# Kernel tuning notes

Measured on AMD Instinct MI355X. Metric: run time of the kernel, lower is better.

Reference implementation:

```python
import jax, jax.numpy as jnp
import numpy as np

HEADS, OUT = 3, 12          # num_heads=3, out_size = output_size*his_num = 12
NEG_SLOPE = 0.2             # PyG GATConv default leaky_relu slope


def gat_layer(y, src, dst, W, a_src, a_dst, bias, concat):
    """One PyG-style GATConv (self-loops already appended to src/dst)."""
    N = y.shape[0]
    h = (y @ W.T).reshape(N, HEADS, OUT)              # [N,H,O]
    al_s = jnp.sum(h * a_src, axis=-1)                # [N,H]
    al_d = jnp.sum(h * a_dst, axis=-1)                # [N,H]
    e = jax.nn.leaky_relu(al_s[src] + al_d[dst], NEG_SLOPE)   # [E,H]
    m = jax.ops.segment_max(e, dst, num_segments=N)
    m = jnp.where(jnp.isfinite(m), m, 0.0)            # guard empty segments
    p = jnp.exp(e - m[dst])
    s = jax.ops.segment_sum(p, dst, num_segments=N)
    alpha = p / (s[dst] + 1e-16)                      # segment softmax
    out = jax.ops.segment_sum(h[src] * alpha[:, :, None], dst, num_segments=N)
    out = out.reshape(N, HEADS * OUT) if concat else out.mean(axis=1)
    return out + bias


def setup_inputs() -> dict:
    key = jax.random.key(0)
    ks = jax.random.split(key, 24)
    B, N, T, C = 1, 50000, 12, 2
    E = 800000
    x = jax.random.normal(ks[0], (B, N, T, C), dtype=jnp.float32)
    edge_index = jax.random.randint(ks[1], (2, E), 0, N, dtype=jnp.int32)
    sc = 0.1
    d = {"x": x, "edge_index": edge_index}
    # layer 0: in=24, layers 1,2: in=36 (concat), layer 3: in=36, concat=False
    ins = [24, 36, 36, 36]
    for l in range(4):
        d[f"W{l}"] = jax.random.normal(ks[2 + 5 * l], (HEADS * OUT, ins[l]), jnp.float32) * sc
        d[f"a_src{l}"] = jax.random.normal(ks[3 + 5 * l], (HEADS, OUT), jnp.float32) * sc
        d[f"a_dst{l}"] = jax.random.normal(ks[4 + 5 * l], (HEADS, OUT), jnp.float32) * sc
        d[f"b{l}"] = jnp.zeros((HEADS * OUT,) if l < 3 else (OUT,), jnp.float32)
    d["lin1_w"] = jax.random.normal(ks[22], (12, 12), jnp.float32) * sc
    d["lin1_b"] = jnp.zeros((12,), jnp.float32)
    d["lin2_w"] = jax.random.normal(ks[23], (6, 12), jnp.float32) * sc
    d["lin2_b"] = jnp.zeros((6,), jnp.float32)
    return d


def reference(x, edge_index, W0, a_src0, a_dst0, b0, W1, a_src1, a_dst1, b1,
              W2, a_src2, a_dst2, b2, W3, a_src3, a_dst3, b3,
              lin1_w, lin1_b, lin2_w, lin2_b):
    b, n, t, c = x.shape
    N = b * n
    y = x.reshape(N, t * c)
    loop = jnp.arange(N, dtype=edge_index.dtype)      # PyG add_self_loops=True
    src = jnp.concatenate([edge_index[0], loop])
    dst = jnp.concatenate([edge_index[1], loop])
    y = jax.nn.relu(gat_layer(y, src, dst, W0, a_src0, a_dst0, b0, True))
    y = jax.nn.relu(gat_layer(y, src, dst, W1, a_src1, a_dst1, b1, True))
    y = jax.nn.relu(gat_layer(y, src, dst, W2, a_src2, a_dst2, b2, True))
    y = gat_layer(y, src, dst, W3, a_src3, a_dst3, b3, False)
    y = y @ lin1_w.T + lin1_b
    y = y @ lin2_w.T + lin2_b
    return y.reshape(b, n, -1)
```

## Files before the change

kernel.cpp:

```cpp
#include <hip/hip_runtime.h>
#include <hip/hip_fp16.h>

#define HEADS 3
#define OUT   12
#define HO    36
#define ROWH  40
#define NMAX  50000
#define CAP   64
#define NPB   28

__device__ __align__(16) unsigned short g_h16A[NMAX * ROWH];
__device__ __align__(16) unsigned short g_h16B[NMAX * ROWH];
__device__ float g_aldA[NMAX * HEADS], g_aldB[NMAX * HEADS];
__device__ int g_pos  [NMAX];
__device__ unsigned short g_elist[NMAX * CAP];

__global__ void scatter_transform24_kernel(const int* __restrict__ ei,
                                           const float* __restrict__ x,
                                           const float* __restrict__ W,
                                           const float* __restrict__ As,
                                           const float* __restrict__ Ad,
                                           int E, int N,
                                           int scatterStart, int scatterBlocks) {
    __shared__ float sW[HO * 24];
    __shared__ float sAs[HO], sAd[HO];
    if (blockIdx.x >= scatterStart) {
        int group = blockIdx.x & 7;
        int bi    = (blockIdx.x - scatterStart) >> 3;
        int range = (N + 7) >> 3;
        int lo = group * range;
        int hi = lo + range; if (hi > N) hi = N;
        int stride = (scatterBlocks >> 3) * 256;
        for (int t = bi * 256 + threadIdx.x; t < E + N; t += stride) {
            int dst = (t < E) ? ei[E + t] : (t - E);
            if (dst < lo || dst >= hi) continue;
            int src = (t < E) ? ei[t] : dst;
            int k = atomicAdd(&g_pos[dst], 1);
            if (k < CAP) g_elist[dst * CAP + k] = (unsigned short)src;
        }
        return;
    }
    for (int i = threadIdx.x; i < HO * 24; i += blockDim.x) sW[i] = W[i];
    if (threadIdx.x < HO) { sAs[threadIdx.x] = As[threadIdx.x]; sAd[threadIdx.x] = Ad[threadIdx.x]; }
    __syncthreads();
    int n = blockIdx.x * blockDim.x + threadIdx.x;
    if (n >= N) return;

    float yv[24];
    const float4* xp = (const float4*)(x + n * 24);
    for (int i = 0; i < 6; ++i) *(float4*)(yv + 4 * i) = xp[i];

    float hr[HO];
    float als[HEADS] = {0.f, 0.f, 0.f};
    float ald[HEADS] = {0.f, 0.f, 0.f};
    for (int ho = 0; ho < HO; ++ho) {
        float acc = 0.f;
#pragma unroll
        for (int k = 0; k < 24; ++k) acc += yv[k] * sW[ho * 24 + k];
        hr[ho] = acc;
        int hd = ho / OUT;
        als[hd] += acc * sAs[ho];
        ald[hd] += acc * sAd[ho];
    }
    unsigned short hp[ROWH];
#pragma unroll
    for (int i = 0; i < HO; ++i) hp[i] = __half_as_ushort(__float2half_rn(hr[i]));
#pragma unroll
    for (int hd = 0; hd < HEADS; ++hd)
        hp[HO + hd] = __half_as_ushort(__float2half_rn(als[hd]));
    hp[ROWH - 1] = 0;
    uint4* dp = (uint4*)(g_h16A + (size_t)n * ROWH);
    const uint4* sp = (const uint4*)hp;
#pragma unroll
    for (int i = 0; i < 5; ++i) dp[i] = sp[i];
    for (int hd = 0; hd < HEADS; ++hd)
        g_aldA[n * HEADS + hd] = ald[hd];
}

__device__ __forceinline__ void gather_row16(int n, int q, int hd,
                                             const unsigned short* __restrict__ hin,
                                             float ald, float4& acc, float& wsum) {
    const unsigned short* row = g_elist + n * CAP;
    int deg = g_pos[n]; if (deg > CAP) deg = CAP;
    const int4* rp = (const int4*)row;
#pragma unroll
    for (int c = 0; c < 4; ++c) {
        if (c * 8 >= deg) break;
        int4 r = rp[c];
#pragma unroll
        for (int j = 0; j < 8; ++j) {
            int s = c * 8 + j;
            if (s < deg) {
                int w2 = (&r.x)[j >> 1];
                int src = (j & 1) ? ((w2 >> 16) & 0xFFFF) : (w2 & 0xFFFF);
                const unsigned short* hrow = hin + (size_t)src * ROWH;
                float als = __half2float(*(const __half*)(hrow + HO + hd));
                float e = als + ald;
                e = (e > 0.f) ? e : 0.2f * e;
                float w = __expf(e);
                wsum += w;
                uint2 hv = *(const uint2*)(hrow + q * 4);
                float2 f0 = __half22float2(*(__half2*)&hv.x);
                float2 f1 = __half22float2(*(__half2*)&hv.y);
                acc.x += w * f0.x; acc.y += w * f0.y;
                acc.z += w * f1.x; acc.w += w * f1.y;
            }
        }
    }
    for (int s = 32; s < deg; ++s) {
        int src = row[s];
        const unsigned short* hrow = hin + (size_t)src * ROWH;
        float als = __half2float(*(const __half*)(hrow + HO + hd));
        float e = als + ald;
        e = (e > 0.f) ? e : 0.2f * e;
        float w = __expf(e);
        wsum += w;
        uint2 hv = *(const uint2*)(hrow + q * 4);
        float2 f0 = __half22float2(*(__half2*)&hv.x);
        float2 f1 = __half22float2(*(__half2*)&hv.y);
        acc.x += w * f0.x; acc.y += w * f0.y;
        acc.z += w * f1.x; acc.w += w * f1.y;
    }
}

__global__ void gather_transform_kernel(const float* __restrict__ bias,
                                        const float* __restrict__ W,
                                        const float* __restrict__ As,
                                        const float* __restrict__ Ad,
                                        int N, int par) {
    const unsigned short* hin = par ? g_h16B : g_h16A;
    const float* aldi = par ? g_aldB : g_aldA;
    unsigned short* hout = par ? g_h16A : g_h16B;
    float* aldo = par ? g_aldA : g_aldB;

    __shared__ float sW[HO * 37];
    __shared__ float sAs[HO], sAd[HO], sB[HO];
    __shared__ float sy[NPB * HO];
    __shared__ float spals[NPB * 9], spald[NPB * 9];

    for (int i = threadIdx.x; i < HO * 36; i += 256) {
        int r = i / 36, c = i - r * 36;
        sW[r * 37 + c] = W[i];
    }
    if (threadIdx.x < HO) {
        sAs[threadIdx.x] = As[threadIdx.x];
        sAd[threadIdx.x] = Ad[threadIdx.x];
        sB[threadIdx.x]  = bias[threadIdx.x];
    }
    __syncthreads();

    int local = threadIdx.x;
    int nodeL = local / 9;
    int q     = local - nodeL * 9;
    int n     = blockIdx.x * NPB + nodeL;
    bool active = (local < NPB * 9) && (n < N);

    if (active) {
        int hd = q / 3;
        float ald = aldi[n * HEADS + hd];
        float4 acc = {0.f, 0.f, 0.f, 0.f};
        float wsum = 0.f;
        gather_row16(n, q, hd, hin, ald, acc, wsum);
        float inv = 1.f / (wsum + 1e-16f);
        float4 v;
        v.x = acc.x * inv + sB[q * 4 + 0];
        v.y = acc.y * inv + sB[q * 4 + 1];
        v.z = acc.z * inv + sB[q * 4 + 2];
        v.w = acc.w * inv + sB[q * 4 + 3];
        v.x = v.x > 0.f ? v.x : 0.f; v.y = v.y > 0.f ? v.y : 0.f;
        v.z = v.z > 0.f ? v.z : 0.f; v.w = v.w > 0.f ? v.w : 0.f;
        *(float4*)(sy + nodeL * HO + q * 4) = v;
    }
    __syncthreads();

    if (active) {
        const float* yv = sy + nodeL * HO;
        float a0 = 0.f, a1 = 0.f, a2 = 0.f, a3 = 0.f;
        const float* w0 = sW + (q * 4 + 0) * 37;
        const float* w1 = sW + (q * 4 + 1) * 37;
        const float* w2 = sW + (q * 4 + 2) * 37;
        const float* w3 = sW + (q * 4 + 3) * 37;
#pragma unroll
        for (int k = 0; k < 36; ++k) {
            float y = yv[k];
            a0 += y * w0[k]; a1 += y * w1[k];
            a2 += y * w2[k]; a3 += y * w3[k];
        }
        __half2 h01 = __floats2half2_rn(a0, a1);
        __half2 h23 = __floats2half2_rn(a2, a3);
        uint2 st;
        st.x = *(unsigned int*)&h01;
        st.y = *(unsigned int*)&h23;
        *(uint2*)(hout + (size_t)n * ROWH + q * 4) = st;
        int r0 = q * 4;
        spals[nodeL * 9 + q] = a0 * sAs[r0] + a1 * sAs[r0 + 1] + a2 * sAs[r0 + 2] + a3 * sAs[r0 + 3];
        spald[nodeL * 9 + q] = a0 * sAd[r0] + a1 * sAd[r0 + 1] + a2 * sAd[r0 + 2] + a3 * sAd[r0 + 3];
    }
    __syncthreads();

    if (active && q < HEADS) {
        float als = spals[nodeL * 9 + q * 3] + spals[nodeL * 9 + q * 3 + 1] + spals[nodeL * 9 + q * 3 + 2];
        float ald = spald[nodeL * 9 + q * 3] + spald[nodeL * 9 + q * 3 + 1] + spald[nodeL * 9 + q * 3 + 2];
        hout[(size_t)n * ROWH + HO + q] = __half_as_ushort(__float2half_rn(als));
        aldo[n * HEADS + q] = ald;
    }
}

__global__ void gather3_finalize_kernel(const float* __restrict__ b3,
                                        const float* __restrict__ lin1_w,
                                        const float* __restrict__ lin1_b,
                                        const float* __restrict__ lin2_w,
                                        const float* __restrict__ lin2_b,
                                        float* __restrict__ out, int N) {
    __shared__ float sv[NPB * HO];
    __shared__ float sl1[144], sl2[72], sl1b[12], sl2b[6], sb3[12];
    if (threadIdx.x < 144) sl1[threadIdx.x] = lin1_w[threadIdx.x];
    if (threadIdx.x < 72)  sl2[threadIdx.x] = lin2_w[threadIdx.x];
    if (threadIdx.x < 12)  { sl1b[threadIdx.x] = lin1_b[threadIdx.x]; sb3[threadIdx.x] = b3[threadIdx.x]; }
    if (threadIdx.x < 6)   sl2b[threadIdx.x] = lin2_b[threadIdx.x];

    int local = threadIdx.x;
    int nodeL = local / 9;
    int q     = local - nodeL * 9;
    int n     = blockIdx.x * NPB + nodeL;
    if (local < NPB * 9 && n < N) {
        int hd = q / 3;
        float ald = g_aldB[n * HEADS + hd];
        float4 acc = {0.f, 0.f, 0.f, 0.f};
        float wsum = 0.f;
        gather_row16(n, q, hd, g_h16B, ald, acc, wsum);
        float inv = 1.f / (wsum + 1e-16f);
        float* s = sv + nodeL * HO + q * 4;
        s[0] = acc.x * inv; s[1] = acc.y * inv;
        s[2] = acc.z * inv; s[3] = acc.w * inv;
    }
    __syncthreads();
    if (local < NPB) {
        int n2 = blockIdx.x * NPB + local;
        if (n2 < N) {
            g_pos[n2] = 0;
            const float* vv = sv + local * HO;
            float v[12];
            for (int o = 0; o < OUT; ++o)
                v[o] = (vv[o] + vv[12 + o] + vv[24 + o]) * (1.f / 3.f) + sb3[o];
            float t1[12];
            for (int i = 0; i < 12; ++i) {
                float a = sl1b[i];
                for (int o = 0; o < 12; ++o) a += v[o] * sl1[i * 12 + o];
                t1[i] = a;
            }
            for (int j = 0; j < 6; ++j) {
                float a = sl2b[j];
                for (int i = 0; i < 12; ++i) a += t1[i] * sl2[j * 12 + i];
                out[n2 * 6 + j] = a;
            }
        }
    }
}

extern "C" void kernel_launch(void* const* d_in, const int* in_sizes, int n_in,
                              void* d_out, int out_size, void* d_ws, size_t ws_size,
                              hipStream_t stream) {
    if (n_in < 22 || d_out == nullptr) return;

    const float* x  = (const float*)d_in[0];
    const int*   ei = (const int*)d_in[1];
    int N = in_sizes[0] / 24;
    int E = in_sizes[1] / 2;
    if (N > NMAX) N = NMAX;

    const float* W[4], *As[4], *Ad[4], *B[4];
    for (int l = 0; l < 4; ++l) {
        W[l]  = (const float*)d_in[2 + 4 * l];
        As[l] = (const float*)d_in[3 + 4 * l];
        Ad[l] = (const float*)d_in[4 + 4 * l];
        B[l]  = (const float*)d_in[5 + 4 * l];
    }
    const float* lin1_w = (const float*)d_in[18];
    const float* lin1_b = (const float*)d_in[19];
    const float* lin2_w = (const float*)d_in[20];
    const float* lin2_b = (const float*)d_in[21];
    float* out = (float*)d_out;

    const int BLK = 256;
    const int nodeBlocks = (N + BLK - 1) / BLK;
    const int scatterStart = ((nodeBlocks + 7) / 8) * 8;
    const int edgeBlocks = (E + N + BLK - 1) / BLK;
    const int scatterBlocks = ((edgeBlocks + 7) / 8) * 8;
    const int fuseBlocks = (N + NPB - 1) / NPB;

    scatter_transform24_kernel<<<scatterStart + scatterBlocks, BLK, 0, stream>>>(
        ei, x, W[0], As[0], Ad[0], E, N, scatterStart, scatterBlocks);
    gather_transform_kernel<<<fuseBlocks, BLK, 0, stream>>>(B[0], W[1], As[1], Ad[1], N, 0);
    gather_transform_kernel<<<fuseBlocks, BLK, 0, stream>>>(B[1], W[2], As[2], Ad[2], N, 1);
    gather_transform_kernel<<<fuseBlocks, BLK, 0, stream>>>(B[2], W[3], As[3], Ad[3], N, 0);
    gather3_finalize_kernel<<<fuseBlocks, BLK, 0, stream>>>(
        B[3], lin1_w, lin1_b, lin2_w, lin2_b, out, N);
}
```

Measured before the change: 227.1 us.

## Sort nodes by degree into a permutation to balance gather work

```diff
diff --git a/kernel.cpp b/kernel.cpp
--- a/kernel.cpp
+++ b/kernel.cpp
@@ -14,19 +14,21 @@
 __device__ float g_aldA[NMAX * HEADS], g_aldB[NMAX * HEADS];
 __device__ int g_pos  [NMAX];
 __device__ unsigned short g_elist[NMAX * CAP];
+__device__ int g_perm [NMAX];
+__device__ int g_dh   [CAP + 1];
+__device__ int g_dcur [CAP + 1];
 
 __global__ void scatter_transform24_kernel(const int* __restrict__ ei,
                                            const float* __restrict__ x,
                                            const float* __restrict__ W,
                                            const float* __restrict__ As,
                                            const float* __restrict__ Ad,
-                                           int E, int N,
-                                           int scatterStart, int scatterBlocks) {
+                                           int E, int N, int scatterBlocks) {
     __shared__ float sW[HO * 24];
     __shared__ float sAs[HO], sAd[HO];
-    if (blockIdx.x >= scatterStart) {
+    if (blockIdx.x < scatterBlocks) {
         int group = blockIdx.x & 7;
-        int bi    = (blockIdx.x - scatterStart) >> 3;
+        int bi    = blockIdx.x >> 3;
         int range = (N + 7) >> 3;
         int lo = group * range;
         int hi = lo + range; if (hi > N) hi = N;
@@ -43,7 +45,7 @@
     for (int i = threadIdx.x; i < HO * 24; i += blockDim.x) sW[i] = W[i];
     if (threadIdx.x < HO) { sAs[threadIdx.x] = As[threadIdx.x]; sAd[threadIdx.x] = Ad[threadIdx.x]; }
     __syncthreads();
-    int n = blockIdx.x * blockDim.x + threadIdx.x;
+    int n = (blockIdx.x - scatterBlocks) * blockDim.x + threadIdx.x;
     if (n >= N) return;
 
     float yv[24];
@@ -75,6 +77,30 @@
     for (int i = 0; i < 5; ++i) dp[i] = sp[i];
     for (int hd = 0; hd < HEADS; ++hd)
         g_aldA[n * HEADS + hd] = ald[hd];
+}
+
+__global__ void degree_hist_kernel(int N) {
+    if (threadIdx.x <= CAP) g_dcur[threadIdx.x] = 0;
+    for (int n = blockIdx.x * blockDim.x + threadIdx.x; n < N;
+         n += gridDim.x * blockDim.x) {
+        int d = g_pos[n]; if (d > CAP) d = CAP;
+        atomicAdd(&g_dh[d], 1);
+    }
+}
+
+__global__ void perm_place_kernel(int N) {
+    __shared__ int sbase[CAP + 1];
+    if (threadIdx.x == 0) {
+        int acc = 0;
+        for (int b = CAP; b >= 0; --b) { sbase[b] = acc; acc += g_dh[b]; }
+    }
+    __syncthreads();
+    for (int n = blockIdx.x * blockDim.x + threadIdx.x; n < N;
+         n += gridDim.x * blockDim.x) {
+        int d = g_pos[n]; if (d > CAP) d = CAP;
+        int off = atomicAdd(&g_dcur[d], 1);
+        g_perm[sbase[d] + off] = n;
+    }
 }
 
 __device__ __forceinline__ void gather_row16(int n, int q, int hd,
@@ -152,8 +178,9 @@
     int local = threadIdx.x;
     int nodeL = local / 9;
     int q     = local - nodeL * 9;
-    int n     = blockIdx.x * NPB + nodeL;
-    bool active = (local < NPB * 9) && (n < N);
+    int idx   = blockIdx.x * NPB + nodeL;
+    bool active = (local < NPB * 9) && (idx < N);
+    int n = active ? g_perm[idx] : 0;
 
     if (active) {
         int hd = q / 3;
@@ -214,16 +241,23 @@
                                         float* __restrict__ out, int N) {
     __shared__ float sv[NPB * HO];
     __shared__ float sl1[144], sl2[72], sl1b[12], sl2b[6], sb3[12];
+    __shared__ int   sperm[NPB];
     if (threadIdx.x < 144) sl1[threadIdx.x] = lin1_w[threadIdx.x];
     if (threadIdx.x < 72)  sl2[threadIdx.x] = lin2_w[threadIdx.x];
     if (threadIdx.x < 12)  { sl1b[threadIdx.x] = lin1_b[threadIdx.x]; sb3[threadIdx.x] = b3[threadIdx.x]; }
     if (threadIdx.x < 6)   sl2b[threadIdx.x] = lin2_b[threadIdx.x];
+    if (threadIdx.x < NPB) {
+        int i2 = blockIdx.x * NPB + threadIdx.x;
+        sperm[threadIdx.x] = (i2 < N) ? g_perm[i2] : 0;
+    }
+    __syncthreads();
 
     int local = threadIdx.x;
     int nodeL = local / 9;
     int q     = local - nodeL * 9;
-    int n     = blockIdx.x * NPB + nodeL;
-    if (local < NPB * 9 && n < N) {
+    int idx   = blockIdx.x * NPB + nodeL;
+    if (local < NPB * 9 && idx < N) {
+        int n = sperm[nodeL];
         int hd = q / 3;
         float ald = g_aldB[n * HEADS + hd];
         float4 acc = {0.f, 0.f, 0.f, 0.f};
@@ -235,10 +269,14 @@
         s[2] = acc.z * inv; s[3] = acc.w * inv;
     }
     __syncthreads();
+    if (blockIdx.x == 0 && threadIdx.x <= CAP) {
+        g_dh[threadIdx.x] = 0; g_dcur[threadIdx.x] = 0;
+    }
     if (local < NPB) {
-        int n2 = blockIdx.x * NPB + local;
-        if (n2 < N) {
-            g_pos[n2] = 0;
+        int idx2 = blockIdx.x * NPB + local;
+        if (idx2 < N) {
+            g_pos[idx2] = 0;
+            int n2 = sperm[local];
             const float* vv = sv + local * HO;
             float v[12];
             for (int o = 0; o < OUT; ++o)
@@ -284,13 +322,14 @@
 
     const int BLK = 256;
     const int nodeBlocks = (N + BLK - 1) / BLK;
-    const int scatterStart = ((nodeBlocks + 7) / 8) * 8;
     const int edgeBlocks = (E + N + BLK - 1) / BLK;
     const int scatterBlocks = ((edgeBlocks + 7) / 8) * 8;
     const int fuseBlocks = (N + NPB - 1) / NPB;
 
-    scatter_transform24_kernel<<<scatterStart + scatterBlocks, BLK, 0, stream>>>(
-        ei, x, W[0], As[0], Ad[0], E, N, scatterStart, scatterBlocks);
+    scatter_transform24_kernel<<<scatterBlocks + nodeBlocks, BLK, 0, stream>>>(
+        ei, x, W[0], As[0], Ad[0], E, N, scatterBlocks);
+    degree_hist_kernel<<<64, BLK, 0, stream>>>(N);
+    perm_place_kernel<<<64, BLK, 0, stream>>>(N);
     gather_transform_kernel<<<fuseBlocks, BLK, 0, stream>>>(B[0], W[1], As[1], Ad[1], N, 0);
     gather_transform_kernel<<<fuseBlocks, BLK, 0, stream>>>(B[1], W[2], As[2], Ad[2], N, 1);
     gather_transform_kernel<<<fuseBlocks, BLK, 0, stream>>>(B[2], W[3], As[3], Ad[3], N, 0);
```

Measured after the change: 486.8 us. +114.4%, slower.
